# Kernel tuning notes

Measured on AMD Instinct MI355X. Metric: run time of the kernel, lower is better.

Reference implementation:

```python
import jax, jax.numpy as jnp
import numpy as np

B, S, D_IN, D_OUT = 4, 2048, 4096, 4096


def setup_inputs() -> dict:
    key = jax.random.key(0)
    k1, k2, k3, k4 = jax.random.split(key, 4)
    x = jax.random.normal(k1, (B, S, D_IN), dtype=jnp.float32) * 0.02
    base = jax.random.normal(k2, (D_IN, D_OUT), dtype=jnp.float32) * 0.02
    # mask holds the sign bits of the weight delta: 1 -> +1, 0 -> -1
    mask = jax.random.randint(k3, (D_IN, D_OUT), 0, 2, dtype=jnp.int32)
    # coeff = mean(|diff|); a small positive scalar
    coeff = jnp.abs(jax.random.normal(k4, (), dtype=jnp.float32)) * 0.01
    return {"x": x, "base": base, "coeff": coeff, "mask": mask}


def reference(x, base, coeff, mask):
    # binary_bmm(x, packed_mask) == x @ sign, sign = 2*mask - 1 in {-1, +1}
    sign = (2 * mask - 1).astype(x.dtype)            # [D_IN, D_OUT]
    return x @ base + coeff * (x @ sign)             # [B, S, D_OUT]
```

## Files before the change

### kernel.cpp

```cpp
#include <hip/hip_runtime.h>
#include <hip/hip_bf16.h>
#include <stdint.h>

#define M_DIM 8192
#define K_DIM 4096
#define N_DIM 4096
#define NT (K_DIM / 64)

typedef __attribute__((ext_vector_type(8))) short short8;
typedef __attribute__((ext_vector_type(4))) float f32x4;
typedef unsigned short ushort_t;

typedef const __attribute__((address_space(1))) unsigned int as1const_u32;
typedef __attribute__((address_space(3))) unsigned int as3_u32;

__device__ __forceinline__ unsigned short f2bf(float f) {
  unsigned int u = __float_as_uint(f);
  u += 0x7FFF + ((u >> 16) & 1);
  return (unsigned short)(u >> 16);
}

__global__ void cvt_x_kernel(const float* __restrict__ x,
                             ushort_t* __restrict__ xb, long n8) {
  long i = (long)blockIdx.x * blockDim.x + threadIdx.x;
  long stride = (long)gridDim.x * blockDim.x;
  for (; i < n8; i += stride) {
    const float4* p = (const float4*)(x + i * 8);
    float4 v0 = p[0], v1 = p[1];
    short8 o;
    o[0] = (short)f2bf(v0.x); o[1] = (short)f2bf(v0.y);
    o[2] = (short)f2bf(v0.z); o[3] = (short)f2bf(v0.w);
    o[4] = (short)f2bf(v1.x); o[5] = (short)f2bf(v1.y);
    o[6] = (short)f2bf(v1.z); o[7] = (short)f2bf(v1.w);
    *(short8*)(xb + i * 8) = o;
  }
}

__global__ void make_wt_kernel(const float* __restrict__ base,
                               const int* __restrict__ mask,
                               const float* __restrict__ coeffp,
                               ushort_t* __restrict__ wt) {
  __shared__ ushort_t tile[32][33];
  const float c = *coeffp;
  const int n0 = blockIdx.x * 32, k0 = blockIdx.y * 32;
  const int tx = threadIdx.x, ty = threadIdx.y;
#pragma unroll
  for (int r = 0; r < 4; ++r) {
    int k = k0 + ty + r * 8;
    int n = n0 + tx;
    size_t idx = (size_t)k * N_DIM + n;
    float s = mask[idx] ? c : -c;
    tile[ty + r * 8][tx] = f2bf(base[idx] + s);
  }
  __syncthreads();
#pragma unroll
  for (int r = 0; r < 4; ++r) {
    int n = n0 + ty + r * 8;
    int k = k0 + tx;
    wt[(size_t)n * K_DIM + k] = tile[tx][ty + r * 8];
  }
}

#define FENCE asm volatile("" ::: "memory")
#define BAR   do { FENCE; __builtin_amdgcn_s_barrier(); FENCE; } while (0)
#define VW8   asm volatile("s_waitcnt vmcnt(8)" ::: "memory")
#define VW0   asm volatile("s_waitcnt vmcnt(0)" ::: "memory")
#define LGK0  asm volatile("s_waitcnt lgkmcnt(0)" ::: "memory")

__global__ __launch_bounds__(512, 2) void gemm_bf16_256(
    const ushort_t* __restrict__ Xb,
    const ushort_t* __restrict__ Wt,
    float* __restrict__ out) {
  __shared__ ushort_t Al[2][256][64];
  __shared__ ushort_t Bl[2][256][64];

  const int tid = threadIdx.x;
  const int lane = tid & 63;
  const int w = tid >> 6;
  const int wm = w >> 2, wn = w & 3;
  const int lrow = lane & 15, kg = lane >> 4;

  const int bid = blockIdx.x;
  const int swz = (bid & 7) * 64 + (bid >> 3);
  const int bm = (swz >> 4) * 256;
  const int bn = (swz & 15) * 256;

  const int rh0 = w * 8 + (lane >> 3);
  const int srcslot = (lane & 7) ^ ((lane >> 3) & 7);
  const ushort_t* Ag = Xb + (size_t)(bm + rh0) * K_DIM + srcslot * 8;
  const ushort_t* Bg = Wt + (size_t)(bn + rh0) * K_DIM + srcslot * 8;
  char* AlB = (char*)&Al[0][0][0];
  char* BlB = (char*)&Bl[0][0][0];
  const int ldsw = w * 1024;

#define STAGE(Og, Lb, u, h) do {                                                   \
    const ushort_t* _s0 = (Og) + (size_t)((h) * 128) * K_DIM + (size_t)(u) * 64;   \
    __builtin_amdgcn_global_load_lds((as1const_u32*)_s0,                           \
        (as3_u32*)((Lb) + ((u) & 1) * 32768 + (h) * 16384 + ldsw), 16, 0, 0);      \
    __builtin_amdgcn_global_load_lds((as1const_u32*)(_s0 + (size_t)64 * K_DIM),    \
        (as3_u32*)((Lb) + ((u) & 1) * 32768 + (h) * 16384 + ldsw + 8192), 16, 0, 0); \
  } while (0)

  const int arow = (wm * 16 + lrow) << 7;
  const int brow = (wn * 16 + lrow) << 7;
  const int sw0 = ((0 + kg) ^ (lrow & 7)) << 4;
  const int sw1 = ((4 + kg) ^ (lrow & 7)) << 4;

#define LDA(bt, mi, kk) (*(const short8*)(AlB + (bt) * 32768 + (mi) * 4096 + arow + ((kk) ? sw1 : sw0)))
#define LDB(bt, ni, kk) (*(const short8*)(BlB + (bt) * 32768 + (ni) * 8192 + brow + ((kk) ? sw1 : sw0)))
#define MFMA(a, b, c) __builtin_amdgcn_mfma_f32_16x16x32_bf16(a, b, c, 0, 0, 0)

  f32x4 acc[8][4] = {};
  short8 Ar0[4][2], Ar1[4][2];
  short8 Br0[2][2], Br1[2][2];

#define RD_A(dst, bt, base)                                                        \
  _Pragma("unroll")                                                                \
  for (int mi = 0; mi < 4; ++mi) {                                                 \
    dst[mi][0] = LDA(bt, (base) + mi, 0); dst[mi][1] = LDA(bt, (base) + mi, 1);    \
  }
#define RD_B(dst, bt, base)                                                        \
  _Pragma("unroll")                                                                \
  for (int ni = 0; ni < 2; ++ni) {                                                 \
    dst[ni][0] = LDB(bt, (base) + ni, 0); dst[ni][1] = LDB(bt, (base) + ni, 1);    \
  }
#define MMQ(mb, nb, Aset, Bset)                                                    \
  _Pragma("unroll")                                                                \
  for (int mi = 0; mi < 4; ++mi)                                                   \
    _Pragma("unroll")                                                              \
    for (int ni = 0; ni < 2; ++ni) {                                               \
      acc[(mb) + mi][(nb) + ni] = MFMA(Aset[mi][0], Bset[ni][0], acc[(mb) + mi][(nb) + ni]); \
      acc[(mb) + mi][(nb) + ni] = MFMA(Aset[mi][1], Bset[ni][1], acc[(mb) + mi][(nb) + ni]); \
    }

  STAGE(Ag, AlB, 0, 0); STAGE(Bg, BlB, 0, 0);
  STAGE(Ag, AlB, 0, 1); STAGE(Bg, BlB, 0, 1);
  STAGE(Ag, AlB, 1, 0); STAGE(Bg, BlB, 1, 0);
  STAGE(Ag, AlB, 1, 1); STAGE(Bg, BlB, 1, 1);
  VW8; BAR;

  for (int t = 0; t < NT - 2; ++t) {
    const int bt = t & 1;

    RD_A(Ar0, bt, 0);
    RD_B(Br0, bt, 0);
    __builtin_amdgcn_s_setprio(1);
    MMQ(0, 0, Ar0, Br0);
    __builtin_amdgcn_s_setprio(0);
    RD_B(Br1, bt, 2);
    RD_A(Ar1, bt, 4);
    __builtin_amdgcn_s_setprio(1);
    MMQ(0, 2, Ar0, Br1);
    __builtin_amdgcn_s_setprio(0);

    LGK0; BAR;
    STAGE(Ag, AlB, t + 2, 0); STAGE(Bg, BlB, t + 2, 0);
    STAGE(Ag, AlB, t + 2, 1); STAGE(Bg, BlB, t + 2, 1);

    __builtin_amdgcn_s_setprio(1);
    MMQ(4, 0, Ar1, Br0);
    MMQ(4, 2, Ar1, Br1);
    __builtin_amdgcn_s_setprio(0);

    VW8; BAR;
  }

  {
    const int bt = (NT - 2) & 1;
    RD_A(Ar0, bt, 0); RD_B(Br0, bt, 0);
    RD_B(Br1, bt, 2); RD_A(Ar1, bt, 4);
    MMQ(0, 0, Ar0, Br0);
    MMQ(0, 2, Ar0, Br1);
    MMQ(4, 0, Ar1, Br0);
    MMQ(4, 2, Ar1, Br1);
  }
  VW0; BAR;
  {
    const int bt = (NT - 1) & 1;
    RD_A(Ar0, bt, 0); RD_B(Br0, bt, 0);
    RD_B(Br1, bt, 2); RD_A(Ar1, bt, 4);
    MMQ(0, 0, Ar0, Br0);
    MMQ(0, 2, Ar0, Br1);
    MMQ(4, 0, Ar1, Br0);
    MMQ(4, 2, Ar1, Br1);
  }

#pragma unroll
  for (int mi = 0; mi < 8; ++mi)
#pragma unroll
    for (int ni = 0; ni < 4; ++ni) {
      const int gr = bm + mi * 32 + wm * 16 + kg * 4;
      const int gc = bn + ni * 64 + wn * 16 + lrow;
      float* o = out + (size_t)gr * N_DIM + gc;
#pragma unroll
      for (int r = 0; r < 4; ++r) o[(size_t)r * N_DIM] = acc[mi][ni][r];
    }
}

__global__ void gemm_f32_fallback(const float* __restrict__ x,
                                  const float* __restrict__ base,
                                  const float* __restrict__ coeffp,
                                  const int* __restrict__ mask,
                                  float* __restrict__ out) {
  __shared__ float As[32][33];
  __shared__ float Bs[32][33];
  const float c = *coeffp;
  const int tx = threadIdx.x, ty = threadIdx.y;
  const int row = blockIdx.y * 32 + ty, col = blockIdx.x * 32 + tx;
  float acc = 0.f;
  for (int kt = 0; kt < K_DIM; kt += 32) {
    As[ty][tx] = x[(size_t)row * K_DIM + kt + tx];
    size_t bidx = (size_t)(kt + ty) * N_DIM + col;
    Bs[ty][tx] = base[bidx] + (mask[bidx] ? c : -c);
    __syncthreads();
#pragma unroll
    for (int k = 0; k < 32; ++k) acc += As[ty][k] * Bs[k][tx];
    __syncthreads();
  }
  out[(size_t)row * N_DIM + col] = acc;
}

extern "C" void kernel_launch(void* const* d_in, const int* in_sizes, int n_in,
                              void* d_out, int out_size, void* d_ws, size_t ws_size,
                              hipStream_t stream) {
  const float* x     = (const float*)d_in[0];
  const float* base  = (const float*)d_in[1];
  const float* coeff = (const float*)d_in[2];
  const int*   mask  = (const int*)d_in[3];
  float* out = (float*)d_out;

  const size_t xb_bytes = (size_t)M_DIM * K_DIM * sizeof(ushort_t);
  const size_t wt_bytes = (size_t)K_DIM * N_DIM * sizeof(ushort_t);

  if (ws_size >= xb_bytes + wt_bytes) {
    ushort_t* xb = (ushort_t*)d_ws;
    ushort_t* wt = (ushort_t*)((char*)d_ws + xb_bytes);
    long n8 = (long)M_DIM * K_DIM / 8;
    cvt_x_kernel<<<4096, 256, 0, stream>>>(x, xb, n8);
    make_wt_kernel<<<dim3(N_DIM / 32, K_DIM / 32), dim3(32, 8), 0, stream>>>(base, mask, coeff, wt);
    gemm_bf16_256<<<512, 512, 0, stream>>>(xb, wt, out);
  } else {
    gemm_f32_fallback<<<dim3(N_DIM / 32, M_DIM / 32), dim3(32, 32), 0, stream>>>(x, base, coeff, mask, out);
  }
}
```

Measured before the change: 330.9 us.

## Interleave global-to-LDS staging with MFMA quarters in an unrolled ping-pong loop

Restructures the GEMM main loop into a two-iteration unrolled schedule. Each of the four MFMA quarters is interleaved with one STAGE of the next tile and bracketed by barriers and priority hints, in the style of an 8-wave ping-pong schedule. Register fragments are reduced to a single A and B set, which lowers VGPR pressure. Global loads now go into LDS halves as soon as each half is consumed, not all at once after a barrier. The cost is many more barriers per tile, and the wait counts and half-buffer reuse must be exactly right to stay correct.

```diff
diff --git a/kernel.cpp b/kernel.cpp
--- a/kernel.cpp
+++ b/kernel.cpp
@@ -63,9 +63,11 @@
 
 #define FENCE asm volatile("" ::: "memory")
 #define BAR   do { FENCE; __builtin_amdgcn_s_barrier(); FENCE; } while (0)
-#define VW8   asm volatile("s_waitcnt vmcnt(8)" ::: "memory")
+#define VW6   asm volatile("s_waitcnt vmcnt(6)" ::: "memory")
 #define VW0   asm volatile("s_waitcnt vmcnt(0)" ::: "memory")
 #define LGK0  asm volatile("s_waitcnt lgkmcnt(0)" ::: "memory")
+#define SP1   __builtin_amdgcn_s_setprio(1)
+#define SP0   __builtin_amdgcn_s_setprio(0)
 
 __global__ __launch_bounds__(512, 2) void gemm_bf16_256(
     const ushort_t* __restrict__ Xb,
@@ -111,79 +113,72 @@
 #define MFMA(a, b, c) __builtin_amdgcn_mfma_f32_16x16x32_bf16(a, b, c, 0, 0, 0)
 
   f32x4 acc[8][4] = {};
-  short8 Ar0[4][2], Ar1[4][2];
-  short8 Br0[2][2], Br1[2][2];
-
-#define RD_A(dst, bt, base)                                                        \
+  short8 Ar[4][2], Br[4][2];
+
+#define RD_A4(bt, base)                                                            \
   _Pragma("unroll")                                                                \
   for (int mi = 0; mi < 4; ++mi) {                                                 \
-    dst[mi][0] = LDA(bt, (base) + mi, 0); dst[mi][1] = LDA(bt, (base) + mi, 1);    \
-  }
-#define RD_B(dst, bt, base)                                                        \
+    Ar[mi][0] = LDA(bt, (base) + mi, 0); Ar[mi][1] = LDA(bt, (base) + mi, 1);      \
+  }
+#define RD_B2(bt, nb)                                                              \
   _Pragma("unroll")                                                                \
   for (int ni = 0; ni < 2; ++ni) {                                                 \
-    dst[ni][0] = LDB(bt, (base) + ni, 0); dst[ni][1] = LDB(bt, (base) + ni, 1);    \
-  }
-#define MMQ(mb, nb, Aset, Bset)                                                    \
+    Br[(nb) + ni][0] = LDB(bt, (nb) + ni, 0); Br[(nb) + ni][1] = LDB(bt, (nb) + ni, 1); \
+  }
+#define MMQ(mb, nb)                                                                \
   _Pragma("unroll")                                                                \
   for (int mi = 0; mi < 4; ++mi)                                                   \
     _Pragma("unroll")                                                              \
     for (int ni = 0; ni < 2; ++ni) {                                               \
-      acc[(mb) + mi][(nb) + ni] = MFMA(Aset[mi][0], Bset[ni][0], acc[(mb) + mi][(nb) + ni]); \
-      acc[(mb) + mi][(nb) + ni] = MFMA(Aset[mi][1], Bset[ni][1], acc[(mb) + mi][(nb) + ni]); \
+      acc[(mb) + mi][(nb) + ni] = MFMA(Ar[mi][0], Br[(nb) + ni][0], acc[(mb) + mi][(nb) + ni]); \
+      acc[(mb) + mi][(nb) + ni] = MFMA(Ar[mi][1], Br[(nb) + ni][1], acc[(mb) + mi][(nb) + ni]); \
     }
 
   STAGE(Ag, AlB, 0, 0); STAGE(Bg, BlB, 0, 0);
-  STAGE(Ag, AlB, 0, 1); STAGE(Bg, BlB, 0, 1);
+  STAGE(Bg, BlB, 0, 1); STAGE(Ag, AlB, 0, 1);
   STAGE(Ag, AlB, 1, 0); STAGE(Bg, BlB, 1, 0);
-  STAGE(Ag, AlB, 1, 1); STAGE(Bg, BlB, 1, 1);
-  VW8; BAR;
-
-  for (int t = 0; t < NT - 2; ++t) {
-    const int bt = t & 1;
-
-    RD_A(Ar0, bt, 0);
-    RD_B(Br0, bt, 0);
-    __builtin_amdgcn_s_setprio(1);
-    MMQ(0, 0, Ar0, Br0);
-    __builtin_amdgcn_s_setprio(0);
-    RD_B(Br1, bt, 2);
-    RD_A(Ar1, bt, 4);
-    __builtin_amdgcn_s_setprio(1);
-    MMQ(0, 2, Ar0, Br1);
-    __builtin_amdgcn_s_setprio(0);
-
-    LGK0; BAR;
-    STAGE(Ag, AlB, t + 2, 0); STAGE(Bg, BlB, t + 2, 0);
-    STAGE(Ag, AlB, t + 2, 1); STAGE(Bg, BlB, t + 2, 1);
-
-    __builtin_amdgcn_s_setprio(1);
-    MMQ(4, 0, Ar1, Br0);
-    MMQ(4, 2, Ar1, Br1);
-    __builtin_amdgcn_s_setprio(0);
-
-    VW8; BAR;
-  }
-
-  {
-    const int bt = (NT - 2) & 1;
-    RD_A(Ar0, bt, 0); RD_B(Br0, bt, 0);
-    RD_B(Br1, bt, 2); RD_A(Ar1, bt, 4);
-    MMQ(0, 0, Ar0, Br0);
-    MMQ(0, 2, Ar0, Br1);
-    MMQ(4, 0, Ar1, Br0);
-    MMQ(4, 2, Ar1, Br1);
-  }
+  STAGE(Bg, BlB, 1, 1);
+  VW6; BAR;
+
+  for (int t = 0; t + 3 < NT; t += 2) {
+    RD_A4(0, 0); RD_B2(0, 0);
+    STAGE(Ag, AlB, t + 1, 1);
+    BAR; LGK0; SP1; MMQ(0, 0); SP0; BAR;
+    RD_B2(0, 2);
+    STAGE(Ag, AlB, t + 2, 0);
+    BAR; LGK0; SP1; MMQ(0, 2); SP0; BAR;
+    RD_A4(0, 4);
+    STAGE(Bg, BlB, t + 2, 0);
+    BAR; LGK0; SP1; MMQ(4, 0); SP0; BAR;
+    STAGE(Bg, BlB, t + 2, 1);
+    BAR; SP1; MMQ(4, 2); SP0; VW6; BAR;
+
+    RD_A4(1, 0); RD_B2(1, 0);
+    STAGE(Ag, AlB, t + 2, 1);
+    BAR; LGK0; SP1; MMQ(0, 0); SP0; BAR;
+    RD_B2(1, 2);
+    STAGE(Ag, AlB, t + 3, 0);
+    BAR; LGK0; SP1; MMQ(0, 2); SP0; BAR;
+    RD_A4(1, 4);
+    STAGE(Bg, BlB, t + 3, 0);
+    BAR; LGK0; SP1; MMQ(4, 0); SP0; BAR;
+    STAGE(Bg, BlB, t + 3, 1);
+    BAR; SP1; MMQ(4, 2); SP0; VW6; BAR;
+  }
+
+  RD_A4(0, 0); RD_B2(0, 0);
+  STAGE(Ag, AlB, NT - 1, 1);
+  BAR; LGK0; SP1; MMQ(0, 0); SP0; BAR;
+  RD_B2(0, 2);
+  BAR; LGK0; SP1; MMQ(0, 2); SP0; BAR;
+  RD_A4(0, 4);
+  BAR; LGK0; SP1; MMQ(4, 0); SP0; BAR;
+  SP1; MMQ(4, 2); SP0;
   VW0; BAR;
-  {
-    const int bt = (NT - 1) & 1;
-    RD_A(Ar0, bt, 0); RD_B(Br0, bt, 0);
-    RD_B(Br1, bt, 2); RD_A(Ar1, bt, 4);
-    MMQ(0, 0, Ar0, Br0);
-    MMQ(0, 2, Ar0, Br1);
-    MMQ(4, 0, Ar1, Br0);
-    MMQ(4, 2, Ar1, Br1);
-  }
+  RD_A4(1, 0); RD_B2(1, 0); RD_B2(1, 2);
+  MMQ(0, 0); MMQ(0, 2);
+  RD_A4(1, 4);
+  MMQ(4, 0); MMQ(4, 2);
 
 #pragma unroll
   for (int mi = 0; mi < 8; ++mi)
```

Result: faster. 312.8 us (-5.5%).
